# Kernel optimization log

Hardware: AMD Instinct MI355X
Metric: run time of the kernel (lower is better)

The kernel has to match this reference:

```python
import jax, jax.numpy as jnp
import numpy as np

NB_BINS = 10
N = 33554432  # number of predictions


def setup_inputs() -> dict:
    key = jax.random.key(0)
    k1, k2 = jax.random.split(key)
    logits = jax.random.normal(k1, (N,), dtype=jnp.float32)
    labels = jax.random.randint(k2, (N,), 0, 2, dtype=jnp.int32)
    return {"logits": logits, "labels": labels}


def reference(logits, labels):
    nb = NB_BINS
    conf = jax.nn.sigmoid(logits)
    # Bin b covers (b/nb, (b+1)/nb]: conf > lower & conf <= upper.
    # ceil(conf*nb)-1 maps exact boundary k/nb to bin k-1, matching gt/le.
    # sigmoid output is strictly in (0,1) for finite logits, so clip is safe.
    bins = jnp.clip(jnp.ceil(conf * nb).astype(jnp.int32) - 1, 0, nb - 1)

    counts = jax.ops.segment_sum(jnp.ones_like(conf), bins, num_segments=nb)
    label_sum = jax.ops.segment_sum(labels.astype(conf.dtype), bins, num_segments=nb)
    conf_sum = jax.ops.segment_sum(conf, bins, num_segments=nb)

    nonempty = counts > 0
    denom = jnp.where(nonempty, counts, 1.0)
    positives_per_bin = jnp.where(nonempty, label_sum / denom, 0.0)
    confidence_per_bin = jnp.where(nonempty, conf_sum / denom, 0.0)

    ece_i = jnp.where(nonempty, jnp.abs(positives_per_bin - confidence_per_bin), 0.0)
    ece = jnp.sum(ece_i)
    max_ece = jnp.max(ece_i)  # original inits max_ece=0, zeros for empty bins match
    return positives_per_bin, confidence_per_bin, ece, max_ece
```

## Files before the change

kernel.cpp:

```cpp
#include <hip/hip_runtime.h>

#define NB 10
#define BLOCK 256
#define GRID 2048
#define SSTRIDE (GRID * BLOCK)


typedef float vfloat4 __attribute__((ext_vector_type(4)));
typedef int   vint4   __attribute__((ext_vector_type(4)));

__device__ __forceinline__ void acc_one(float xx, unsigned ll,
                                        unsigned long long& cnt64,
                                        unsigned long long& lab64,
                                        unsigned long long& rA,
                                        unsigned long long& rB) {
    float e = __expf(-xx);
    float t = __builtin_amdgcn_rcpf(__builtin_fmaf(e, 0.1f, 0.1f));
    int b = (int)t;
    b = min(b, NB - 1);
    float r = t - (float)b;
    unsigned rfix = (unsigned)__builtin_fmaf(r, 63.0f, 0.5f);
    int s6 = b * 6;
    cnt64 += 1ULL << s6;
    lab64 += (unsigned long long)ll << s6;
    bool hi = b >= 5;
    int s12 = (hi ? b - 5 : b) * 12;
    unsigned long long val = (unsigned long long)rfix << s12;
    rA += hi ? 0ULL : val;
    rB += hi ? val : 0ULL;
}

__device__ __forceinline__ void flush_packed(unsigned long long& cnt64,
                                             unsigned long long& lab64,
                                             unsigned long long& rA,
                                             unsigned long long& rB,
                                             unsigned* cl, unsigned* ru) {
#pragma unroll
    for (int i = 0; i < NB; ++i) {
        unsigned c = (unsigned)((cnt64 >> (6 * i)) & 63ULL);
        unsigned l = (unsigned)((lab64 >> (6 * i)) & 63ULL);
        cl[i] += c | (l << 16);
    }
#pragma unroll
    for (int i = 0; i < 5; ++i) {
        ru[i]     += (unsigned)((rA >> (12 * i)) & 4095ULL);
        ru[5 + i] += (unsigned)((rB >> (12 * i)) & 4095ULL);
    }
    cnt64 = 0ULL; lab64 = 0ULL; rA = 0ULL; rB = 0ULL;
}

__global__ __launch_bounds__(BLOCK, 2) void ece_partial(const float* __restrict__ logits,
                                                        const int* __restrict__ labels,
                                                        unsigned int* __restrict__ ws,
                                                        int n, int wstride) {
    const int tid = threadIdx.x;
    const int gtid = blockIdx.x * BLOCK + tid;
    const int n4 = n >> 2;
    const vfloat4* __restrict__ l4 = (const vfloat4*)logits;
    const vint4*   __restrict__ b4 = (const vint4*)labels;

    unsigned cl[NB], ru[NB];
#pragma unroll
    for (int i = 0; i < NB; ++i) { cl[i] = 0u; ru[i] = 0u; }

    if (n4 == 16 * SSTRIDE) {
        vfloat4 x0[8], x1[8];
        vint4   y0[8], y1[8];
#pragma unroll
        for (int j = 0; j < 8; ++j) x0[j] = __builtin_nontemporal_load(&l4[gtid + j * SSTRIDE]);
#pragma unroll
        for (int j = 0; j < 8; ++j) y0[j] = __builtin_nontemporal_load(&b4[gtid + j * SSTRIDE]);
#pragma unroll
        for (int j = 0; j < 8; ++j) x1[j] = __builtin_nontemporal_load(&l4[gtid + (8 + j) * SSTRIDE]);
#pragma unroll
        for (int j = 0; j < 8; ++j) y1[j] = __builtin_nontemporal_load(&b4[gtid + (8 + j) * SSTRIDE]);
        __builtin_amdgcn_sched_barrier(0);

        unsigned long long cnt64 = 0ULL, lab64 = 0ULL, rA = 0ULL, rB = 0ULL;
#pragma unroll
        for (int j = 0; j < 8; ++j) {
#pragma unroll
            for (int k = 0; k < 4; ++k)
                acc_one(x0[j][k], (unsigned)y0[j][k], cnt64, lab64, rA, rB);
        }
        flush_packed(cnt64, lab64, rA, rB, cl, ru);
#pragma unroll
        for (int j = 0; j < 8; ++j) {
#pragma unroll
            for (int k = 0; k < 4; ++k)
                acc_one(x1[j][k], (unsigned)y1[j][k], cnt64, lab64, rA, rB);
        }
        flush_packed(cnt64, lab64, rA, rB, cl, ru);
    } else {
        for (int v = gtid; v < n4; v += SSTRIDE) {
            unsigned long long cnt64 = 0ULL, lab64 = 0ULL, rA = 0ULL, rB = 0ULL;
            vfloat4 x = __builtin_nontemporal_load(&l4[v]);
            vint4   y = __builtin_nontemporal_load(&b4[v]);
#pragma unroll
            for (int k = 0; k < 4; ++k)
                acc_one(x[k], (unsigned)y[k], cnt64, lab64, rA, rB);
            flush_packed(cnt64, lab64, rA, rB, cl, ru);
        }
        if (gtid == 0 && (n & 3)) {
            unsigned long long cnt64 = 0ULL, lab64 = 0ULL, rA = 0ULL, rB = 0ULL;
            for (int j2 = n4 * 4; j2 < n; ++j2)
                acc_one(logits[j2], (unsigned)labels[j2], cnt64, lab64, rA, rB);
            flush_packed(cnt64, lab64, rA, rB, cl, ru);
        }
    }

#pragma unroll
    for (int i = 0; i < NB; ++i) {
#pragma unroll
        for (int off = 32; off > 0; off >>= 1) {
            cl[i] += __shfl_down(cl[i], off, 64);
            ru[i] += __shfl_down(ru[i], off, 64);
        }
    }

    __shared__ unsigned red[4][2 * NB];
    const int wave = tid >> 6, lane = tid & 63;
    if (lane == 0) {
#pragma unroll
        for (int i = 0; i < NB; ++i) { red[wave][i] = cl[i]; red[wave][NB + i] = ru[i]; }
    }
    __syncthreads();
    if (tid < 2 * NB) {
        unsigned s = red[0][tid] + red[1][tid] + red[2][tid] + red[3][tid];
        if (tid < NB) {
            atomicAdd(&ws[tid * wstride], s & 0xffffu);
            atomicAdd(&ws[(NB + tid) * wstride], s >> 16);
        } else {
            atomicAdd(&ws[(NB + tid) * wstride], s);
        }
    }
}

__global__ void ece_final(const unsigned int* __restrict__ ws, float* __restrict__ out,
                          int wstride) {
    if (threadIdx.x == 0 && blockIdx.x == 0) {
        float ece = 0.0f, mx = 0.0f;
        for (int b = 0; b < NB; ++b) {
            unsigned cnt = ws[b * wstride];
            unsigned lab = ws[(NB + b) * wstride];
            unsigned rs  = ws[(2 * NB + b) * wstride];
            float pos = 0.0f, cfb = 0.0f, e = 0.0f;
            if (cnt > 0u) {
                float inv = 1.0f / (float)cnt;
                pos = (float)lab * inv;
                cfb = ((float)b + (float)rs * (1.0f / 63.0f) * inv) * 0.1f;
                e = fabsf(pos - cfb);
            }
            out[b] = pos;
            out[NB + b] = cfb;
            ece += e;
            mx = fmaxf(mx, e);
        }
        out[2 * NB] = ece;
        out[2 * NB + 1] = mx;
    }
}

extern "C" void kernel_launch(void* const* d_in, const int* in_sizes, int n_in,
                              void* d_out, int out_size, void* d_ws, size_t ws_size,
                              hipStream_t stream) {
    const float* logits = (const float*)d_in[0];
    const int*   labels = (const int*)d_in[1];
    float* out = (float*)d_out;
    unsigned int* ws = (unsigned int*)d_ws;
    int n = in_sizes[0];

    int wstride = (ws_size >= 30 * 16 * sizeof(unsigned)) ? 16 : 1;
    hipMemsetAsync(d_ws, 0, (size_t)(30 * wstride) * sizeof(unsigned), stream);

    ece_partial<<<GRID, BLOCK, 0, stream>>>(logits, labels, ws, n, wstride);
    ece_final<<<1, 64, 0, stream>>>(ws, out, wstride);
}
```

Baseline: 275.6 us.

## Double-buffer loads in fast path and raise occupancy to four blocks per SIMD

Replaces the up-front load of all 32 vectors per thread with a two-stage double buffer that prefetches the next 4 logit/label vectors while the current 4 are processed. This cuts register pressure, which allows raising the launch-bounds occupancy hint from 2 to 4. It also computes the fractional remainder with floorf instead of the clamped bin index. The trade-off is less memory-level parallelism per thread, offset by more resident waves. The floorf change alters results for the top clamp case, where t reaches 10.

```diff
diff --git a/kernel.cpp b/kernel.cpp
--- a/kernel.cpp
+++ b/kernel.cpp
@@ -18,7 +18,7 @@
     float t = __builtin_amdgcn_rcpf(__builtin_fmaf(e, 0.1f, 0.1f));
     int b = (int)t;
     b = min(b, NB - 1);
-    float r = t - (float)b;
+    float r = t - floorf(t);
     unsigned rfix = (unsigned)__builtin_fmaf(r, 63.0f, 0.5f);
     int s6 = b * 6;
     cnt64 += 1ULL << s6;
@@ -49,7 +49,7 @@
     cnt64 = 0ULL; lab64 = 0ULL; rA = 0ULL; rB = 0ULL;
 }
 
-__global__ __launch_bounds__(BLOCK, 2) void ece_partial(const float* __restrict__ logits,
+__global__ __launch_bounds__(BLOCK, 4) void ece_partial(const float* __restrict__ logits,
                                                         const int* __restrict__ labels,
                                                         unsigned int* __restrict__ ws,
                                                         int n, int wstride) {
@@ -64,33 +64,32 @@
     for (int i = 0; i < NB; ++i) { cl[i] = 0u; ru[i] = 0u; }
 
     if (n4 == 16 * SSTRIDE) {
-        vfloat4 x0[8], x1[8];
-        vint4   y0[8], y1[8];
+        vfloat4 xb[2][4];
+        vint4   yb[2][4];
 #pragma unroll
-        for (int j = 0; j < 8; ++j) x0[j] = __builtin_nontemporal_load(&l4[gtid + j * SSTRIDE]);
-#pragma unroll
-        for (int j = 0; j < 8; ++j) y0[j] = __builtin_nontemporal_load(&b4[gtid + j * SSTRIDE]);
-#pragma unroll
-        for (int j = 0; j < 8; ++j) x1[j] = __builtin_nontemporal_load(&l4[gtid + (8 + j) * SSTRIDE]);
-#pragma unroll
-        for (int j = 0; j < 8; ++j) y1[j] = __builtin_nontemporal_load(&b4[gtid + (8 + j) * SSTRIDE]);
-        __builtin_amdgcn_sched_barrier(0);
-
+        for (int j = 0; j < 4; ++j) {
+            xb[0][j] = __builtin_nontemporal_load(&l4[gtid + j * SSTRIDE]);
+            yb[0][j] = __builtin_nontemporal_load(&b4[gtid + j * SSTRIDE]);
+        }
         unsigned long long cnt64 = 0ULL, lab64 = 0ULL, rA = 0ULL, rB = 0ULL;
 #pragma unroll
-        for (int j = 0; j < 8; ++j) {
+        for (int it = 0; it < 4; ++it) {
+            const int cur = it & 1, nxt = cur ^ 1;
+            if (it < 3) {
 #pragma unroll
-            for (int k = 0; k < 4; ++k)
-                acc_one(x0[j][k], (unsigned)y0[j][k], cnt64, lab64, rA, rB);
+                for (int j = 0; j < 4; ++j) {
+                    xb[nxt][j] = __builtin_nontemporal_load(&l4[gtid + ((it + 1) * 4 + j) * SSTRIDE]);
+                    yb[nxt][j] = __builtin_nontemporal_load(&b4[gtid + ((it + 1) * 4 + j) * SSTRIDE]);
+                }
+            }
+#pragma unroll
+            for (int j = 0; j < 4; ++j) {
+#pragma unroll
+                for (int k = 0; k < 4; ++k)
+                    acc_one(xb[cur][j][k], (unsigned)yb[cur][j][k], cnt64, lab64, rA, rB);
+            }
+            if (it & 1) flush_packed(cnt64, lab64, rA, rB, cl, ru);
         }
-        flush_packed(cnt64, lab64, rA, rB, cl, ru);
-#pragma unroll
-        for (int j = 0; j < 8; ++j) {
-#pragma unroll
-            for (int k = 0; k < 4; ++k)
-                acc_one(x1[j][k], (unsigned)y1[j][k], cnt64, lab64, rA, rB);
-        }
-        flush_packed(cnt64, lab64, rA, rB, cl, ru);
     } else {
         for (int v = gtid; v < n4; v += SSTRIDE) {
             unsigned long long cnt64 = 0ULL, lab64 = 0ULL, rA = 0ULL, rB = 0ULL;
```

New measurement: 282.2 us. 1.02x slower.
